# Performance work log

Hardware: AMD Instinct MI355X
Metric: run time of the kernel (lower is better)

Reference implementation:

```python
import jax, jax.numpy as jnp
import numpy as np

B, S, HID, NH = 4, 1024, 1024, 16
DK = HID // NH
SCALE = DK ** -0.5
NEG = -9e15


def setup_inputs() -> dict:
    key = jax.random.key(0)
    ks = jax.random.split(key, 10)
    std = HID ** -0.5
    return {
        "batch": jax.random.normal(ks[0], (B, S, HID), jnp.float32),
        "attn_bias": jax.random.normal(ks[1], (B, NH, S, S), jnp.float32),
        "Wq": jax.random.normal(ks[2], (HID, HID), jnp.float32) * std,
        "bq": jnp.zeros((HID,), jnp.float32),
        "Wk": jax.random.normal(ks[3], (HID, HID), jnp.float32) * std,
        "bk": jnp.zeros((HID,), jnp.float32),
        "Wv": jax.random.normal(ks[4], (HID, HID), jnp.float32) * std,
        "bv": jnp.zeros((HID,), jnp.float32),
        "Wo": jax.random.normal(ks[5], (HID, HID), jnp.float32) * std,
        "bo": jnp.zeros((HID,), jnp.float32),
    }


def reference(batch, attn_bias, Wq, bq, Wk, bk, Wv, bv, Wo, bo):
    b, s, _ = batch.shape
    # QKV projections -> [b, h, s, d]
    q = (batch @ Wq.T + bq).reshape(b, s, NH, DK).transpose(0, 2, 1, 3)
    k = (batch @ Wk.T + bk).reshape(b, s, NH, DK).transpose(0, 2, 1, 3)
    v = (batch @ Wv.T + bv).reshape(b, s, NH, DK).transpose(0, 2, 1, 3)
    # scaled scores [b, h, s, s]
    x = jnp.einsum("bhqd,bhkd->bhqk", q * SCALE, k)
    # custom zero-mask: exact zeros become -9e15
    x = jnp.where(x == 0, jnp.float32(NEG), x)
    x = x + attn_bias
    p = jax.nn.softmax(x, axis=3)  # dropout_rate=0.0 -> identity
    o = jnp.einsum("bhqk,bhkd->bhqd", p, v)
    o = o.transpose(0, 2, 1, 3).reshape(b, s, NH * DK)
    return o @ Wo.T + bo
```

## Files before the change

kernel.cpp:

```cpp
#include <hip/hip_runtime.h>
#include <hip/hip_bf16.h>
#include <stdint.h>
#include <stddef.h>

#define Bd  4
#define Sd  1024
#define Hd  1024
#define NHd 16
#define DKd 64
#define SCALEF 0.125f
#define NEGV  -9.0e15f
#define L2E   1.4426950408889634f

typedef __attribute__((ext_vector_type(8))) short bfrag;
typedef __attribute__((ext_vector_type(4))) float facc;
typedef __attribute__((ext_vector_type(4))) float f32x4;

typedef __attribute__((address_space(1))) const unsigned int ga_u32;
typedef __attribute__((address_space(3))) unsigned int ls_u32;

__device__ __forceinline__ void gload_lds16(const void* g, void* l) {
  __builtin_amdgcn_global_load_lds((ga_u32*)g, (ls_u32*)l, 16, 0, 0);
}

__device__ __forceinline__ unsigned short f2bf(float f) {
  unsigned int u = __float_as_uint(f);
  u += 0x7fffu + ((u >> 16) & 1u);
  return (unsigned short)(u >> 16);
}

__global__ void castk_all(const float* __restrict__ s0, const float* __restrict__ s1,
                          const float* __restrict__ s2, const float* __restrict__ s3,
                          const float* __restrict__ s4,
                          unsigned short* __restrict__ d0, unsigned short* __restrict__ d1,
                          unsigned short* __restrict__ d2, unsigned short* __restrict__ d3,
                          unsigned short* __restrict__ d4) {
  const int id = blockIdx.x;
  const float* s; unsigned short* d; int i;
  if (id < 4096) { s = s0; d = d0; i = id * 256 + threadIdx.x; }
  else {
    const int w = (id - 4096) >> 10;
    s = (w == 0) ? s1 : (w == 1) ? s2 : (w == 2) ? s3 : s4;
    d = (w == 0) ? d1 : (w == 1) ? d2 : (w == 2) ? d3 : d4;
    i = ((id - 4096) & 1023) * 256 + threadIdx.x;
  }
  float4 v = ((const float4*)s)[i];
  ushort4 ov;
  ov.x = f2bf(v.x); ov.y = f2bf(v.y); ov.z = f2bf(v.z); ov.w = f2bf(v.w);
  ((ushort4*)d)[i] = ov;
}

__global__ __launch_bounds__(256, 3)
void gemm_qkv(const unsigned short* __restrict__ A,
              const unsigned short* __restrict__ W0, const unsigned short* __restrict__ W1,
              const unsigned short* __restrict__ W2,
              const float* __restrict__ b0, const float* __restrict__ b1, const float* __restrict__ b2,
              unsigned short* __restrict__ o0, unsigned short* __restrict__ o1, unsigned short* __restrict__ o2) {
  __shared__ __align__(16) unsigned short smem[128 * 136];
  unsigned short* sA = smem;
  unsigned short* sB = smem + 4096;
  const int z = blockIdx.z;
  const unsigned short* Bm = (z == 0) ? W0 : (z == 1) ? W1 : W2;
  const float* bias = (z == 0) ? b0 : (z == 1) ? b1 : b2;
  unsigned short* out = (z == 0) ? o0 : (z == 1) ? o1 : o2;

  const int m0 = blockIdx.x * 128, n0 = blockIdx.y * 128;
  const int tid = threadIdx.x;
  const int wave = tid >> 6, lane = tid & 63;
  const int quad = lane >> 4, l16 = lane & 15;
  const int wm = wave >> 1, wn = wave & 1;

  facc acc[4][4] = {};

  const int j0 = wave * 128 + lane;
  const int j1 = j0 + 64;
  const int row0 = j0 >> 2, ko0 = (j0 & 3) << 3;
  const int row1 = j1 >> 2, ko1 = (j1 & 3) << 3;
  const size_t aoff0 = (size_t)(m0 + row0) * 1024 + ko0;
  const size_t aoff1 = (size_t)(m0 + row1) * 1024 + ko1;
  const size_t boff0 = (size_t)(n0 + row0) * 1024 + ko0;
  const size_t boff1 = (size_t)(n0 + row1) * 1024 + ko1;
  unsigned short* sA0 = sA + (wave * 2 + 0) * 512;
  unsigned short* sA1 = sA + (wave * 2 + 1) * 512;
  unsigned short* sB0 = sB + (wave * 2 + 0) * 512;
  unsigned short* sB1 = sB + (wave * 2 + 1) * 512;

  for (int k0 = 0; k0 < 1024; k0 += 32) {
    gload_lds16(A + aoff0 + k0, sA0);
    gload_lds16(A + aoff1 + k0, sA1);
    gload_lds16(Bm + boff0 + k0, sB0);
    gload_lds16(Bm + boff1 + k0, sB1);
    __syncthreads();
    bfrag af[4], bf[4];
#pragma unroll
    for (int i = 0; i < 4; ++i) af[i] = *(const bfrag*)(sA + (wm * 64 + i * 16 + l16) * 32 + quad * 8);
#pragma unroll
    for (int j = 0; j < 4; ++j) bf[j] = *(const bfrag*)(sB + (wn * 64 + j * 16 + l16) * 32 + quad * 8);
#pragma unroll
    for (int i = 0; i < 4; ++i)
#pragma unroll
      for (int j = 0; j < 4; ++j)
        acc[i][j] = __builtin_amdgcn_mfma_f32_16x16x32_bf16(af[i], bf[j], acc[i][j], 0, 0, 0);
    __syncthreads();
  }

  if (z < 2) {
#pragma unroll
    for (int i = 0; i < 4; ++i)
#pragma unroll
      for (int j = 0; j < 4; ++j) {
        const int col = n0 + wn * 64 + j * 16 + l16;
        const float bv = bias[col];
        const int h = col >> 6, d = col & 63;
#pragma unroll
        for (int r = 0; r < 4; ++r) {
          const int m = m0 + wm * 64 + i * 16 + quad * 4 + r;
          const int b = m >> 10, s = m & 1023;
          out[(((size_t)(b * NHd + h) * Sd) + s) * DKd + d] = f2bf(acc[i][j][r] + bv);
        }
      }
  } else {
    unsigned short* sT = smem;
#pragma unroll
    for (int i = 0; i < 4; ++i)
#pragma unroll
      for (int j = 0; j < 4; ++j) {
        const int col = n0 + wn * 64 + j * 16 + l16;
        const float bv = bias[col];
        const int nrow = wn * 64 + j * 16 + l16;
        const int mbase = wm * 64 + i * 16 + quad * 4;
        ushort4 pk;
        pk.x = f2bf(acc[i][j][0] + bv);
        pk.y = f2bf(acc[i][j][1] + bv);
        pk.z = f2bf(acc[i][j][2] + bv);
        pk.w = f2bf(acc[i][j][3] + bv);
        *(ushort4*)(sT + nrow * 136 + mbase) = pk;
      }
    __syncthreads();
    const int bI = m0 >> 10, s0i = m0 & 1023;
#pragma unroll
    for (int it = 0; it < 8; ++it) {
      const int c = tid + it * 256;
      const int row = c >> 4, mc = (c & 15) * 8;
      bfrag vv = *(const bfrag*)(sT + row * 136 + mc);
      const int col = n0 + row, hh = col >> 6, dd = col & 63;
      *(bfrag*)(out + (((size_t)(bI * NHd + hh) * DKd) + dd) * Sd + s0i + mc) = vv;
    }
  }
}

__global__ __launch_bounds__(256, 3)
void gemm_out(const unsigned short* __restrict__ A, const unsigned short* __restrict__ Bm,
              const float* __restrict__ bias, float* __restrict__ out) {
  __shared__ __align__(16) unsigned short sA[64 * 64];
  __shared__ __align__(16) unsigned short sB[128 * 64];
  const int m0 = blockIdx.x * 64, n0 = blockIdx.y * 128;
  const int tid = threadIdx.x;
  const int wave = tid >> 6, lane = tid & 63;
  const int quad = lane >> 4, l16 = lane & 15;

  facc acc[8] = {};

  const int cA0 = (wave * 2 + 0) * 64 + lane;
  const int cA1 = (wave * 2 + 1) * 64 + lane;
  const int rA0 = cA0 >> 3, kA0 = ((cA0 & 7) ^ (rA0 & 7)) * 8;
  const int rA1 = cA1 >> 3, kA1 = ((cA1 & 7) ^ (rA1 & 7)) * 8;
  const size_t aoff0 = (size_t)(m0 + rA0) * 1024 + kA0;
  const size_t aoff1 = (size_t)(m0 + rA1) * 1024 + kA1;
  size_t boff[4];
#pragma unroll
  for (int i = 0; i < 4; ++i) {
    const int c = (wave * 4 + i) * 64 + lane;
    const int r = c >> 3, kk = ((c & 7) ^ (r & 7)) * 8;
    boff[i] = (size_t)(n0 + r) * 1024 + kk;
  }

  for (int k0 = 0; k0 < 1024; k0 += 64) {
    gload_lds16(A + aoff0 + k0, sA + (wave * 2 + 0) * 512);
    gload_lds16(A + aoff1 + k0, sA + (wave * 2 + 1) * 512);
#pragma unroll
    for (int i = 0; i < 4; ++i)
      gload_lds16(Bm + boff[i] + k0, sB + (wave * 4 + i) * 512);
    __syncthreads();
#pragma unroll
    for (int c2 = 0; c2 < 2; ++c2) {
      const int ko = ((c2 * 4 + quad) ^ (l16 & 7)) * 8;
      bfrag af = *(const bfrag*)(sA + (wave * 16 + l16) * 64 + ko);
#pragma unroll
      for (int j = 0; j < 8; ++j) {
        bfrag bf = *(const bfrag*)(sB + (j * 16 + l16) * 64 + ko);
        acc[j] = __builtin_amdgcn_mfma_f32_16x16x32_bf16(af, bf, acc[j], 0, 0, 0);
      }
    }
    __syncthreads();
  }

#pragma unroll
  for (int j = 0; j < 8; ++j) {
    const int col = n0 + j * 16 + l16;
    const float bv = bias[col];
#pragma unroll
    for (int r = 0; r < 4; ++r) {
      const int m = m0 + wave * 16 + quad * 4 + r;
      out[(size_t)m * 1024 + col] = acc[j][r] + bv;
    }
  }
}

__global__ __attribute__((amdgpu_flat_work_group_size(128, 128), amdgpu_waves_per_eu(4, 4)))
void attn_kernel(const unsigned short* __restrict__ q,
                 const unsigned short* __restrict__ k,
                 const unsigned short* __restrict__ vt,
                 const float* __restrict__ bias,
                 unsigned short* __restrict__ o)
{
  __shared__ __align__(16) unsigned int sP[2][16][36];
  const int p = blockIdx.x;
  const int xcd = p & 7;
  const int g = p >> 3;
  const int bh = ((g >> 5) << 3) | xcd;
  const int q0 = (g & 31) * 32;
  const int tid = threadIdx.x;
  const int wave = tid >> 6, lane = tid & 63;
  const int quad = lane >> 4, l16 = lane & 15;
  const int b = bh >> 4, h = bh & 15;

  const unsigned short* qh = q + (size_t)bh * Sd * DKd;
  const unsigned short* kh = k + (size_t)bh * Sd * DKd;
  const unsigned short* vh = vt + (size_t)bh * DKd * Sd;
  const float* bias_h = bias + (size_t)bh * Sd * Sd;
  const int rq = q0 + wave * 16;
  unsigned int (*sPw)[36] = sP[wave];

  bfrag qf[2];
#pragma unroll
  for (int c = 0; c < 2; ++c)
    qf[c] = *(const bfrag*)(qh + (size_t)(rq + l16) * DKd + c * 32 + quad * 8);

  facc oacc[4] = {};
  float lsum = 0.f;
  const float SL2 = SCALEF * L2E;

  const float* bpS = bias_h + (size_t)(rq + l16) * Sd + quad * 4;
  f32x4 br0 = __builtin_nontemporal_load((const f32x4*)(bpS + 0));
  f32x4 br1 = __builtin_nontemporal_load((const f32x4*)(bpS + 16));
  f32x4 br2 = __builtin_nontemporal_load((const f32x4*)(bpS + 32));
  f32x4 br3 = __builtin_nontemporal_load((const f32x4*)(bpS + 48));

  for (int t = 0; t < 16; ++t) {
    const int k0 = t * 64;
    facc sacc[4] = {};
#pragma unroll
    for (int c = 0; c < 2; ++c)
#pragma unroll
      for (int j = 0; j < 4; ++j) {
        bfrag kf = *(const bfrag*)(kh + (size_t)(k0 + j * 16 + l16) * DKd + c * 32 + quad * 8);
        sacc[j] = __builtin_amdgcn_mfma_f32_16x16x32_bf16(kf, qf[c], sacc[j], 0, 0, 0);
      }
    asm volatile("" : "+v"(br0), "+v"(br1), "+v"(br2), "+v"(br3));
    unsigned int pk[4][2];
#pragma unroll
    for (int j = 0; j < 4; ++j) {
      const f32x4 bb = (j == 0) ? br0 : (j == 1) ? br1 : (j == 2) ? br2 : br3;
      float e0 = __builtin_amdgcn_exp2f(fmaf(sacc[j][0], SL2, bb.x * L2E));
      float e1 = __builtin_amdgcn_exp2f(fmaf(sacc[j][1], SL2, bb.y * L2E));
      float e2 = __builtin_amdgcn_exp2f(fmaf(sacc[j][2], SL2, bb.z * L2E));
      float e3 = __builtin_amdgcn_exp2f(fmaf(sacc[j][3], SL2, bb.w * L2E));
      e0 = (sacc[j][0] == 0.f) ? 0.f : e0;
      e1 = (sacc[j][1] == 0.f) ? 0.f : e1;
      e2 = (sacc[j][2] == 0.f) ? 0.f : e2;
      e3 = (sacc[j][3] == 0.f) ? 0.f : e3;
      lsum += (e0 + e1) + (e2 + e3);
      pk[j][0] = (unsigned int)f2bf(e0) | ((unsigned int)f2bf(e1) << 16);
      pk[j][1] = (unsigned int)f2bf(e2) | ((unsigned int)f2bf(e3) << 16);
    }
    if (t < 15) {
      const float* bpn = bpS + k0 + 64;
      br0 = __builtin_nontemporal_load((const f32x4*)(bpn + 0));
      br1 = __builtin_nontemporal_load((const f32x4*)(bpn + 16));
      br2 = __builtin_nontemporal_load((const f32x4*)(bpn + 32));
      br3 = __builtin_nontemporal_load((const f32x4*)(bpn + 48));
    }
#pragma unroll
    for (int j = 0; j < 4; ++j) {
      uint2 w; w.x = pk[j][0]; w.y = pk[j][1];
      *(uint2*)&sPw[l16][j * 8 + quad * 2] = w;
    }
#pragma unroll
    for (int c = 0; c < 2; ++c) {
      bfrag pf = *(const bfrag*)&sPw[l16][c * 16 + quad * 4];
#pragma unroll
      for (int n = 0; n < 4; ++n) {
        bfrag vf = *(const bfrag*)(vh + (size_t)(n * 16 + l16) * Sd + k0 + c * 32 + quad * 8);
        oacc[n] = __builtin_amdgcn_mfma_f32_16x16x32_bf16(vf, pf, oacc[n], 0, 0, 0);
      }
    }
  }

  lsum += __shfl_xor(lsum, 16, 64);
  lsum += __shfl_xor(lsum, 32, 64);
  const float rinv = 1.0f / lsum;

  const size_t rowo = (size_t)(b * Sd + rq + l16) * Hd + h * 64 + quad * 4;
#pragma unroll
  for (int n = 0; n < 4; ++n) {
    ushort4 st;
    st.x = f2bf(oacc[n][0] * rinv);
    st.y = f2bf(oacc[n][1] * rinv);
    st.z = f2bf(oacc[n][2] * rinv);
    st.w = f2bf(oacc[n][3] * rinv);
    *(ushort4*)(o + rowo + n * 16) = st;
  }
}

extern "C" void kernel_launch(void* const* d_in, const int* in_sizes, int n_in,
                              void* d_out, int out_size, void* d_ws, size_t ws_size,
                              hipStream_t stream) {
  const float* batch = (const float*)d_in[0];
  const float* attn_bias = (const float*)d_in[1];
  const float* Wq = (const float*)d_in[2];
  const float* bq = (const float*)d_in[3];
  const float* Wk = (const float*)d_in[4];
  const float* bk = (const float*)d_in[5];
  const float* Wv = (const float*)d_in[6];
  const float* bv = (const float*)d_in[7];
  const float* Wo = (const float*)d_in[8];
  const float* bo = (const float*)d_in[9];
  float* out = (float*)d_out;

  unsigned short* ws = (unsigned short*)d_ws;
  unsigned short* Ab  = ws;
  unsigned short* Wqb = Ab  + 4194304;
  unsigned short* Wkb = Wqb + 1048576;
  unsigned short* Wvb = Wkb + 1048576;
  unsigned short* Wob = Wvb + 1048576;
  unsigned short* qb  = Wob + 1048576;
  unsigned short* kb  = qb  + 4194304;
  unsigned short* vtb = kb  + 4194304;
  unsigned short* ob  = vtb + 4194304;

  castk_all<<<8192, 256, 0, stream>>>(batch, Wq, Wk, Wv, Wo, Ab, Wqb, Wkb, Wvb, Wob);
  gemm_qkv<<<dim3(32, 8, 3), 256, 0, stream>>>(Ab, Wqb, Wkb, Wvb, bq, bk, bv, qb, kb, vtb);
  attn_kernel<<<dim3(2048), 128, 0, stream>>>(qb, kb, vtb, attn_bias, ob);
  gemm_out<<<dim3(64, 8), 256, 0, stream>>>(ob, Wob, bo, out);
}
```

Baseline: 536.7 us.

## Split attention KV range across two wave pairs and reduce partials in LDS

Each attention block now runs four waves: two handle the query halves and two handle the key/value halves (split-K over 512 keys each). Partial output accumulators and row sums from the second KV half are stored to shared memory and merged by the first half before normalisation and store. This doubles wave-level parallelism per block to better hide the bias-load and exp latency, at the cost of extra LDS traffic, a block barrier, and idle waves during the final reduction. The no-max softmax makes the simple sum-merge valid.

```diff
diff --git a/kernel.cpp b/kernel.cpp
--- a/kernel.cpp
+++ b/kernel.cpp
@@ -207,14 +207,16 @@
   }
 }
 
-__global__ __attribute__((amdgpu_flat_work_group_size(128, 128), amdgpu_waves_per_eu(4, 4)))
+__global__ __attribute__((amdgpu_flat_work_group_size(256, 256), amdgpu_waves_per_eu(8)))
 void attn_kernel(const unsigned short* __restrict__ q,
                  const unsigned short* __restrict__ k,
                  const unsigned short* __restrict__ vt,
                  const float* __restrict__ bias,
                  unsigned short* __restrict__ o)
 {
-  __shared__ __align__(16) unsigned int sP[2][16][36];
+  __shared__ __align__(16) unsigned int sP[4][16][36];
+  __shared__ __align__(16) float sO[2][16][68];
+  __shared__ float sL[2][16];
   const int p = blockIdx.x;
   const int xcd = p & 7;
   const int g = p >> 3;
@@ -222,6 +224,7 @@
   const int q0 = (g & 31) * 32;
   const int tid = threadIdx.x;
   const int wave = tid >> 6, lane = tid & 63;
+  const int qhalf = wave & 1, kvhalf = wave >> 1;
   const int quad = lane >> 4, l16 = lane & 15;
   const int b = bh >> 4, h = bh & 15;
 
@@ -229,7 +232,8 @@
   const unsigned short* kh = k + (size_t)bh * Sd * DKd;
   const unsigned short* vh = vt + (size_t)bh * DKd * Sd;
   const float* bias_h = bias + (size_t)bh * Sd * Sd;
-  const int rq = q0 + wave * 16;
+  const int rq = q0 + qhalf * 16;
+  const int kvbase = kvhalf * 512;
   unsigned int (*sPw)[36] = sP[wave];
 
   bfrag qf[2];
@@ -241,14 +245,15 @@
   float lsum = 0.f;
   const float SL2 = SCALEF * L2E;
 
-  const float* bpS = bias_h + (size_t)(rq + l16) * Sd + quad * 4;
+  const float* bpS = bias_h + (size_t)(rq + l16) * Sd + kvbase + quad * 4;
   f32x4 br0 = __builtin_nontemporal_load((const f32x4*)(bpS + 0));
   f32x4 br1 = __builtin_nontemporal_load((const f32x4*)(bpS + 16));
   f32x4 br2 = __builtin_nontemporal_load((const f32x4*)(bpS + 32));
   f32x4 br3 = __builtin_nontemporal_load((const f32x4*)(bpS + 48));
 
-  for (int t = 0; t < 16; ++t) {
-    const int k0 = t * 64;
+  for (int t = 0; t < 8; ++t) {
+    const int koff = t * 64;
+    const int k0 = kvbase + koff;
     facc sacc[4] = {};
 #pragma unroll
     for (int c = 0; c < 2; ++c)
@@ -274,8 +279,8 @@
       pk[j][0] = (unsigned int)f2bf(e0) | ((unsigned int)f2bf(e1) << 16);
       pk[j][1] = (unsigned int)f2bf(e2) | ((unsigned int)f2bf(e3) << 16);
     }
-    if (t < 15) {
-      const float* bpn = bpS + k0 + 64;
+    if (t < 7) {
+      const float* bpn = bpS + koff + 64;
       br0 = __builtin_nontemporal_load((const f32x4*)(bpn + 0));
       br1 = __builtin_nontemporal_load((const f32x4*)(bpn + 16));
       br2 = __builtin_nontemporal_load((const f32x4*)(bpn + 32));
@@ -299,17 +304,32 @@
 
   lsum += __shfl_xor(lsum, 16, 64);
   lsum += __shfl_xor(lsum, 32, 64);
-  const float rinv = 1.0f / lsum;
-
-  const size_t rowo = (size_t)(b * Sd + rq + l16) * Hd + h * 64 + quad * 4;
-#pragma unroll
-  for (int n = 0; n < 4; ++n) {
-    ushort4 st;
-    st.x = f2bf(oacc[n][0] * rinv);
-    st.y = f2bf(oacc[n][1] * rinv);
-    st.z = f2bf(oacc[n][2] * rinv);
-    st.w = f2bf(oacc[n][3] * rinv);
-    *(ushort4*)(o + rowo + n * 16) = st;
+
+  if (kvhalf) {
+#pragma unroll
+    for (int n = 0; n < 4; ++n)
+      *(facc*)&sO[qhalf][l16][n * 16 + quad * 4] = oacc[n];
+    if (quad == 0) sL[qhalf][l16] = lsum;
+  }
+  __syncthreads();
+  if (!kvhalf) {
+    lsum += sL[qhalf][l16];
+    const float rinv = 1.0f / lsum;
+#pragma unroll
+    for (int n = 0; n < 4; ++n) {
+      const facc op = *(const facc*)&sO[qhalf][l16][n * 16 + quad * 4];
+      oacc[n] += op;
+    }
+    const size_t rowo = (size_t)(b * Sd + rq + l16) * Hd + h * 64 + quad * 4;
+#pragma unroll
+    for (int n = 0; n < 4; ++n) {
+      ushort4 st;
+      st.x = f2bf(oacc[n][0] * rinv);
+      st.y = f2bf(oacc[n][1] * rinv);
+      st.z = f2bf(oacc[n][2] * rinv);
+      st.w = f2bf(oacc[n][3] * rinv);
+      *(ushort4*)(o + rowo + n * 16) = st;
+    }
   }
 }
 
@@ -341,6 +361,6 @@
 
   castk_all<<<8192, 256, 0, stream>>>(batch, Wq, Wk, Wv, Wo, Ab, Wqb, Wkb, Wvb, Wob);
   gemm_qkv<<<dim3(32, 8, 3), 256, 0, stream>>>(Ab, Wqb, Wkb, Wvb, bq, bk, bv, qb, kb, vtb);
-  attn_kernel<<<dim3(2048), 128, 0, stream>>>(qb, kb, vtb, attn_bias, ob);
+  attn_kernel<<<dim3(2048), 256, 0, stream>>>(qb, kb, vtb, attn_bias, ob);
   gemm_out<<<dim3(64, 8), 256, 0, stream>>>(ob, Wob, bo, out);
 }
```

Result: slower. 651.5 us (+21.4%).

## Stage K/V tiles in LDS shared across eight waves with double buffering

Applied to the files above, without the earlier changes.

The attention kernel grows from 2-wave blocks covering 32 query rows to 8-wave blocks covering 128 query rows, with 512 blocks instead of 2048. Each 64-key tile of K and V^T is loaded once per block into XOR-swizzled, double-buffered LDS using async global-to-LDS loads, and the MFMA fragments are read from there instead of directly from global memory by every wave. This cuts redundant K/V global traffic and lets the next tile load overlap compute, at the cost of a block-wide barrier every iteration and fewer, larger blocks.

```diff
diff --git a/kernel.cpp b/kernel.cpp
--- a/kernel.cpp
+++ b/kernel.cpp
@@ -207,19 +207,22 @@
   }
 }
 
-__global__ __attribute__((amdgpu_flat_work_group_size(128, 128), amdgpu_waves_per_eu(4, 4)))
+__global__ __attribute__((amdgpu_flat_work_group_size(512, 512), amdgpu_waves_per_eu(4, 4)))
 void attn_kernel(const unsigned short* __restrict__ q,
                  const unsigned short* __restrict__ k,
                  const unsigned short* __restrict__ vt,
                  const float* __restrict__ bias,
                  unsigned short* __restrict__ o)
 {
-  __shared__ __align__(16) unsigned int sP[2][16][36];
+  __shared__ __align__(16) unsigned short sK[2][64 * 64];
+  __shared__ __align__(16) unsigned short sV[2][64 * 64];
+  __shared__ __align__(16) unsigned int sP[8][16][36];
+
   const int p = blockIdx.x;
   const int xcd = p & 7;
   const int g = p >> 3;
-  const int bh = ((g >> 5) << 3) | xcd;
-  const int q0 = (g & 31) * 32;
+  const int bh = ((g >> 3) << 3) | xcd;
+  const int qblk = g & 7;
   const int tid = threadIdx.x;
   const int wave = tid >> 6, lane = tid & 63;
   const int quad = lane >> 4, l16 = lane & 15;
@@ -229,8 +232,20 @@
   const unsigned short* kh = k + (size_t)bh * Sd * DKd;
   const unsigned short* vh = vt + (size_t)bh * DKd * Sd;
   const float* bias_h = bias + (size_t)bh * Sd * Sd;
-  const int rq = q0 + wave * 16;
+  const int rq = qblk * 128 + wave * 16;
   unsigned int (*sPw)[36] = sP[wave];
+
+  const int srow = wave * 8 + (lane >> 3);
+  const int sslot = (lane & 7) ^ (srow & 7);
+  const unsigned short* srcK = kh + (size_t)srow * DKd + sslot * 8;
+  const unsigned short* srcV = vh + (size_t)srow * Sd + sslot * 8;
+  unsigned short* dK0 = sK[0] + wave * 512;
+  unsigned short* dK1 = sK[1] + wave * 512;
+  unsigned short* dV0 = sV[0] + wave * 512;
+  unsigned short* dV1 = sV[1] + wave * 512;
+
+  const int xs0 = ((0 + quad) ^ (l16 & 7)) * 8;
+  const int xs1 = ((4 + quad) ^ (l16 & 7)) * 8;
 
   bfrag qf[2];
 #pragma unroll
@@ -247,25 +262,39 @@
   f32x4 br2 = __builtin_nontemporal_load((const f32x4*)(bpS + 32));
   f32x4 br3 = __builtin_nontemporal_load((const f32x4*)(bpS + 48));
 
+  gload_lds16(srcK, dK0);
+  gload_lds16(srcV, dV0);
+  __syncthreads();
+
   for (int t = 0; t < 16; ++t) {
-    const int k0 = t * 64;
+    const int bb = t & 1;
+    if (t < 15) {
+      const int kn = (t + 1) * 64;
+      gload_lds16(srcK + (size_t)kn * DKd, bb ? dK0 : dK1);
+      gload_lds16(srcV + kn, bb ? dV0 : dV1);
+    }
+    const unsigned short* sKb = sK[bb];
+    const unsigned short* sVb = sV[bb];
     facc sacc[4] = {};
 #pragma unroll
-    for (int c = 0; c < 2; ++c)
-#pragma unroll
-      for (int j = 0; j < 4; ++j) {
-        bfrag kf = *(const bfrag*)(kh + (size_t)(k0 + j * 16 + l16) * DKd + c * 32 + quad * 8);
-        sacc[j] = __builtin_amdgcn_mfma_f32_16x16x32_bf16(kf, qf[c], sacc[j], 0, 0, 0);
-      }
+    for (int j = 0; j < 4; ++j) {
+      bfrag kf = *(const bfrag*)(sKb + (j * 16 + l16) * 64 + xs0);
+      sacc[j] = __builtin_amdgcn_mfma_f32_16x16x32_bf16(kf, qf[0], sacc[j], 0, 0, 0);
+    }
+#pragma unroll
+    for (int j = 0; j < 4; ++j) {
+      bfrag kf = *(const bfrag*)(sKb + (j * 16 + l16) * 64 + xs1);
+      sacc[j] = __builtin_amdgcn_mfma_f32_16x16x32_bf16(kf, qf[1], sacc[j], 0, 0, 0);
+    }
     asm volatile("" : "+v"(br0), "+v"(br1), "+v"(br2), "+v"(br3));
     unsigned int pk[4][2];
 #pragma unroll
     for (int j = 0; j < 4; ++j) {
-      const f32x4 bb = (j == 0) ? br0 : (j == 1) ? br1 : (j == 2) ? br2 : br3;
-      float e0 = __builtin_amdgcn_exp2f(fmaf(sacc[j][0], SL2, bb.x * L2E));
-      float e1 = __builtin_amdgcn_exp2f(fmaf(sacc[j][1], SL2, bb.y * L2E));
-      float e2 = __builtin_amdgcn_exp2f(fmaf(sacc[j][2], SL2, bb.z * L2E));
-      float e3 = __builtin_amdgcn_exp2f(fmaf(sacc[j][3], SL2, bb.w * L2E));
+      const f32x4 bv = (j == 0) ? br0 : (j == 1) ? br1 : (j == 2) ? br2 : br3;
+      float e0 = __builtin_amdgcn_exp2f(fmaf(sacc[j][0], SL2, bv.x * L2E));
+      float e1 = __builtin_amdgcn_exp2f(fmaf(sacc[j][1], SL2, bv.y * L2E));
+      float e2 = __builtin_amdgcn_exp2f(fmaf(sacc[j][2], SL2, bv.z * L2E));
+      float e3 = __builtin_amdgcn_exp2f(fmaf(sacc[j][3], SL2, bv.w * L2E));
       e0 = (sacc[j][0] == 0.f) ? 0.f : e0;
       e1 = (sacc[j][1] == 0.f) ? 0.f : e1;
       e2 = (sacc[j][2] == 0.f) ? 0.f : e2;
@@ -275,7 +304,7 @@
       pk[j][1] = (unsigned int)f2bf(e2) | ((unsigned int)f2bf(e3) << 16);
     }
     if (t < 15) {
-      const float* bpn = bpS + k0 + 64;
+      const float* bpn = bpS + (t + 1) * 64;
       br0 = __builtin_nontemporal_load((const f32x4*)(bpn + 0));
       br1 = __builtin_nontemporal_load((const f32x4*)(bpn + 16));
       br2 = __builtin_nontemporal_load((const f32x4*)(bpn + 32));
@@ -289,12 +318,14 @@
 #pragma unroll
     for (int c = 0; c < 2; ++c) {
       bfrag pf = *(const bfrag*)&sPw[l16][c * 16 + quad * 4];
+      const int xsc = c ? xs1 : xs0;
 #pragma unroll
       for (int n = 0; n < 4; ++n) {
-        bfrag vf = *(const bfrag*)(vh + (size_t)(n * 16 + l16) * Sd + k0 + c * 32 + quad * 8);
+        bfrag vf = *(const bfrag*)(sVb + (n * 16 + l16) * 64 + xsc);
         oacc[n] = __builtin_amdgcn_mfma_f32_16x16x32_bf16(vf, pf, oacc[n], 0, 0, 0);
       }
     }
+    __syncthreads();
   }
 
   lsum += __shfl_xor(lsum, 16, 64);
@@ -341,6 +372,6 @@
 
   castk_all<<<8192, 256, 0, stream>>>(batch, Wq, Wk, Wv, Wo, Ab, Wqb, Wkb, Wvb, Wob);
   gemm_qkv<<<dim3(32, 8, 3), 256, 0, stream>>>(Ab, Wqb, Wkb, Wvb, bq, bk, bv, qb, kb, vtb);
-  attn_kernel<<<dim3(2048), 128, 0, stream>>>(qb, kb, vtb, attn_bias, ob);
+  attn_kernel<<<dim3(512), 512, 0, stream>>>(qb, kb, vtb, attn_bias, ob);
   gemm_out<<<dim3(64, 8), 256, 0, stream>>>(ob, Wob, bo, out);
 }
```

After: 452.2 us. -15.7%, faster.
